# Performance work log

Measured on AMD Instinct MI355X. Metric: run time of the kernel, lower is better.

## Reference

```python
import jax, jax.numpy as jnp
import numpy as np
from jax import lax

WEIGHT = 1.0
NUM_DILATION_STEPS = 20
FAR_DIST = 20.0


def _neighbor_count(x, kernel, num_classes):
    # grouped 3x3 conv with center tap zeroed, SAME padding (stride 1)
    return lax.conv_general_dilated(
        x, kernel, window_strides=(1, 1), padding='SAME',
        feature_group_count=num_classes,
        dimension_numbers=('NCHW', 'OIHW', 'NCHW'))


def fast_sdf(target_mask, num_classes):
    # target_mask: [B, H, W] int labels -> per-class chamfer-ish distance map [B, C, H, W]
    one_hot = jnp.transpose(jax.nn.one_hot(target_mask, num_classes, dtype=jnp.float32),
                            (0, 3, 1, 2))  # [B, C, H, W]
    foreground = (one_hot > 0.5).astype(jnp.float32)

    # 3x3 all-ones kernel with center zero, one per class (grouped conv)
    k = np.ones((num_classes, 1, 3, 3), dtype=np.float32)
    k[:, 0, 1, 1] = 0.0
    kernel = jnp.asarray(k)

    dist_map0 = jnp.zeros_like(foreground)

    def step(i, state):
        dist_map, current_mask = state
        dilated = (_neighbor_count(current_mask, kernel, num_classes) > 0).astype(jnp.float32)
        # note: faithful to torch code -- pixels with no neighbors vanish and
        # contribute negative increments, exactly as `dilated - current_mask` does
        new_pixels = dilated - current_mask
        dist_map = dist_map + new_pixels * (i + 1).astype(jnp.float32)
        return (dist_map, dilated)

    dist_map, current_mask = lax.fori_loop(0, NUM_DILATION_STEPS, step,
                                           (dist_map0, foreground))
    return jnp.where(current_mask == 0, FAR_DIST, dist_map)


def setup_inputs() -> dict:
    key = jax.random.key(0)
    k1, k2 = jax.random.split(key)
    B, C, H, W = 8, 19, 512, 512
    pred = jax.random.normal(k1, (B, C, H, W), dtype=jnp.float32)
    target = jax.random.randint(k2, (B, H, W), 0, C, dtype=jnp.int64)
    return {"pred": pred, "target": target}


def reference(pred, target):
    num_classes = pred.shape[1]
    probs = jax.nn.softmax(pred, axis=1)
    gt_sdf = lax.stop_gradient(fast_sdf(target, num_classes))
    loss = jnp.mean(probs * gt_sdf)
    return WEIGHT * loss
```

## Files before the change

### kernel.cpp

```cpp
#include <hip/hip_runtime.h>

#define B_ 8
#define C_ 19
#define H_ 512
#define W_ 512
#define HW_ (H_*W_)

#define HALO   20
#define INTR   8
#define WIN    48
#define NSTRIP 64

typedef unsigned long long u64;

__global__ __launch_bounds__(256) void mask_kernel(const int* __restrict__ target,
                                                   u64* __restrict__ masks) {
    __shared__ u64 mlds[64][21];
    const int blk  = blockIdx.x;
    const int b    = blk >> 6;
    const int base = (blk & 63) * 64;
    const int tid  = threadIdx.x;
    const int lane = tid & 63, wv = tid >> 6;
    const int* tgt = target + b * HW_;
    for (int t = 0; t < 16; ++t) {
        const int cl = wv * 16 + t;
        const int x  = tgt[(base + cl) * 64 + lane];
        u64 keep = 0;
        #pragma unroll
        for (int c = 0; c < C_; ++c) {
            u64 m = __ballot(x == c);
            if (lane == c) keep = m;
        }
        if (lane < C_) mlds[cl][lane] = keep;
    }
    __syncthreads();
    for (int idx = tid; idx < C_ * 64; idx += 256) {
        const int c = idx >> 6, wl = idx & 63;
        masks[((size_t)b * C_ + c) * 4096 + base + wl] = mlds[wl][c];
    }
}

__global__ __launch_bounds__(256, 2) void fused_kernel(const u64* __restrict__ masks,
                                                       const float* __restrict__ pred,
                                                       float* __restrict__ out) {
    __shared__ unsigned char sdfl[C_ * INTR * W_];
    __shared__ float part[4];
    const int blk   = blockIdx.x;
    const int strip = blk & 63;
    const int b     = blk >> 6;
    const int tid   = threadIdx.x;
    const int wv    = tid >> 6, lane = tid & 63;
    const int w     = lane & 7, g = lane >> 3;
    const int gytop = strip * INTR - HALO;

    for (int c = wv; c < C_; c += 4) {
        const u64* mk = masks + ((size_t)b * C_ + c) * 4096;
        u64 cov[6], h[6], iso[6], pl[6][5];

        #pragma unroll
        for (int i = 0; i < 6; ++i) {
            const int gy = gytop + g * 6 + i;
            cov[i] = (gy >= 0 && gy < H_) ? mk[gy * 8 + w] : 0;
            iso[i] = 0;
            #pragma unroll
            for (int j = 0; j < 5; ++j) pl[i][j] = 0;
        }

        u64 nc[6];
        {
            unsigned mp = 0, lp = 0;
            #pragma unroll
            for (int i = 0; i < 6; ++i) {
                mp |= (unsigned)(cov[i] >> 63) << i;
                lp |= ((unsigned)cov[i] & 1) << i;
            }
            unsigned fl = __shfl_up(mp, 1);   if (w == 0) fl = 0;
            unsigned fr = __shfl_down(lp, 1); if (w == 7) fr = 0;
            #pragma unroll
            for (int i = 0; i < 6; ++i) {
                nc[i] = (cov[i] << 1) | (cov[i] >> 1) | (u64)((fl >> i) & 1) | ((u64)((fr >> i) & 1) << 63);
                h[i]  = nc[i] | cov[i];
            }
        }

        bool active;
        {
            u64 hup = __shfl_up(h[5], 8);   if (g == 0) hup = 0;
            u64 hdn = __shfl_down(h[0], 8); if (g == 7) hdn = 0;
            u64 d[6], diffw = 0;
            #pragma unroll
            for (int i = 0; i < 6; ++i) {
                const u64 up  = (i > 0) ? h[i - 1] : hup;
                const u64 dn  = (i < 5) ? h[i + 1] : hdn;
                const u64 nbr = nc[i] | up | dn;
                iso[i] = cov[i] & ~nbr;
                const u64 nb = nbr & ~cov[i];
                pl[i][0] = nb;
                d[i] = cov[i] | nbr;
                diffw |= nb;
                cov[i] = d[i];
            }
            unsigned mp = 0, lp = 0;
            #pragma unroll
            for (int i = 0; i < 6; ++i) {
                mp |= (unsigned)(cov[i] >> 63) << i;
                lp |= ((unsigned)cov[i] & 1) << i;
            }
            unsigned fl = __shfl_up(mp, 1);   if (w == 0) fl = 0;
            unsigned fr = __shfl_down(lp, 1); if (w == 7) fr = 0;
            #pragma unroll
            for (int i = 0; i < 6; ++i)
                h[i] = cov[i] | (cov[i] << 1) | (cov[i] >> 1) | (u64)((fl >> i) & 1) | ((u64)((fr >> i) & 1) << 63);
            active = __any(diffw != 0);
        }

        if (active) {
            #pragma unroll
            for (int s = 2; s <= 19; ++s) {
                u64 hup = __shfl_up(h[5], 8);   if (g == 0) hup = 0;
                u64 hdn = __shfl_down(h[0], 8); if (g == 7) hdn = 0;
                u64 diffw = 0;
                #pragma unroll
                for (int i = 0; i < 6; ++i) {
                    const u64 up = (i > 0) ? h[i - 1] : hup;
                    const u64 dn = (i < 5) ? h[i + 1] : hdn;
                    const u64 d  = up | h[i] | dn;
                    const u64 nb = d ^ cov[i];
                    diffw |= nb;
                    if (s & 1)  pl[i][0] |= nb;
                    if (s & 2)  pl[i][1] |= nb;
                    if (s & 4)  pl[i][2] |= nb;
                    if (s & 8)  pl[i][3] |= nb;
                    if (s & 16) pl[i][4] |= nb;
                    cov[i] = d;
                }
                if (!__any(diffw != 0)) break;
                if (s < 19) {
                    unsigned mp = 0, lp = 0;
                    #pragma unroll
                    for (int i = 0; i < 6; ++i) {
                        mp |= (unsigned)(cov[i] >> 63) << i;
                        lp |= ((unsigned)cov[i] & 1) << i;
                    }
                    unsigned fl = __shfl_up(mp, 1);   if (w == 0) fl = 0;
                    unsigned fr = __shfl_down(lp, 1); if (w == 7) fr = 0;
                    #pragma unroll
                    for (int i = 0; i < 6; ++i)
                        h[i] = cov[i] | (cov[i] << 1) | (cov[i] >> 1) | (u64)((fl >> i) & 1) | ((u64)((fr >> i) & 1) << 63);
                }
            }
        }

        #pragma unroll
        for (int i = 0; i < 6; ++i) {
            const int lr = g * 6 + i;
            if (lr < HALO || lr >= HALO + INTR) continue;
            pl[i][0] |= iso[i];
            const u64 m = ~cov[i];
            pl[i][2] |= m;
            pl[i][4] |= m;
            u64* dst = (u64*)&sdfl[(c * INTR + (lr - HALO)) * W_ + w * 64];
            #pragma unroll
            for (int g2 = 0; g2 < 8; ++g2) {
                u64 x = 0;
                #pragma unroll
                for (int j = 0; j < 5; ++j)
                    x |= ((pl[i][j] >> (8 * g2)) & 0xFFULL) << (8 * j);
                u64 t;
                t = (x ^ (x >> 7))  & 0x00AA00AA00AA00AAULL; x ^= t ^ (t << 7);
                t = (x ^ (x >> 14)) & 0x0000CCCC0000CCCCULL; x ^= t ^ (t << 14);
                t = (x ^ (x >> 28)) & 0x00000000F0F0F0F0ULL; x ^= t ^ (t << 28);
                dst[g2] = x;
            }
        }
    }
    __syncthreads();

    float acc = 0.f;
    const float* pb = pred + (size_t)b * C_ * HW_ + (size_t)strip * INTR * W_;
    #pragma unroll
    for (int k = 0; k < 4; ++k) {
        const int p = k * 1024 + tid * 4;
        float4 den = {0.f, 0.f, 0.f, 0.f};
        float4 num = {0.f, 0.f, 0.f, 0.f};
        #pragma unroll
        for (int c = 0; c < C_; ++c) {
            const float4 v  = *(const float4*)(pb + (size_t)c * HW_ + p);
            const uchar4 sv = *(const uchar4*)&sdfl[c * 4096 + p];
            const float e0 = __expf(v.x), e1 = __expf(v.y);
            const float e2 = __expf(v.z), e3 = __expf(v.w);
            den.x += e0; den.y += e1; den.z += e2; den.w += e3;
            num.x = fmaf(e0, (float)sv.x, num.x);
            num.y = fmaf(e1, (float)sv.y, num.y);
            num.z = fmaf(e2, (float)sv.z, num.z);
            num.w = fmaf(e3, (float)sv.w, num.w);
        }
        acc += num.x / den.x + num.y / den.y + num.z / den.z + num.w / den.w;
    }

    #pragma unroll
    for (int off = 32; off > 0; off >>= 1) acc += __shfl_down(acc, off);
    if ((tid & 63) == 0) part[tid >> 6] = acc;
    __syncthreads();
    if (tid == 0) {
        float s = (part[0] + part[1]) + (part[2] + part[3]);
        atomicAdd(out, s * (1.0f / 39845888.0f));
    }
}

extern "C" void kernel_launch(void* const* d_in, const int* in_sizes, int n_in,
                              void* d_out, int out_size, void* d_ws, size_t ws_size,
                              hipStream_t stream) {
    const float* pred   = (const float*)d_in[0];
    const int*   target = (const int*)d_in[1];
    u64* masks = (u64*)d_ws;
    float* out = (float*)d_out;

    hipMemsetAsync(out, 0, sizeof(float), stream);
    mask_kernel<<<512, 256, 0, stream>>>(target, masks);
    fused_kernel<<<B_ * NSTRIP, 256, 0, stream>>>(masks, pred, out);
}
```

Measured before the change: 277.4 us.

## Split fused dilation+loss kernel into separate dilate and loss kernels

New measurement: 300.2 us. 8.2% more time.

```diff
diff --git a/kernel.cpp b/kernel.cpp
--- a/kernel.cpp
+++ b/kernel.cpp
@@ -8,7 +8,6 @@
 
 #define HALO   20
 #define INTR   8
-#define WIN    48
 #define NSTRIP 64
 
 typedef unsigned long long u64;
@@ -40,169 +39,161 @@
     }
 }
 
-__global__ __launch_bounds__(256, 2) void fused_kernel(const u64* __restrict__ masks,
-                                                       const float* __restrict__ pred,
-                                                       float* __restrict__ out) {
-    __shared__ unsigned char sdfl[C_ * INTR * W_];
-    __shared__ float part[4];
-    const int blk   = blockIdx.x;
-    const int strip = blk & 63;
-    const int b     = blk >> 6;
-    const int tid   = threadIdx.x;
-    const int wv    = tid >> 6, lane = tid & 63;
+__global__ __launch_bounds__(256) void dilate_kernel(const u64* __restrict__ masks,
+                                                     unsigned char* __restrict__ sdf) {
+    const int wid   = blockIdx.x * 4 + (threadIdx.x >> 6);
+    const int strip = wid & 63;
+    const int bc    = wid >> 6;
+    const int lane  = threadIdx.x & 63;
     const int w     = lane & 7, g = lane >> 3;
     const int gytop = strip * INTR - HALO;
-
-    for (int c = wv; c < C_; c += 4) {
-        const u64* mk = masks + ((size_t)b * C_ + c) * 4096;
-        u64 cov[6], h[6], iso[6], pl[6][5];
-
-        #pragma unroll
-        for (int i = 0; i < 6; ++i) {
-            const int gy = gytop + g * 6 + i;
-            cov[i] = (gy >= 0 && gy < H_) ? mk[gy * 8 + w] : 0;
-            iso[i] = 0;
-            #pragma unroll
-            for (int j = 0; j < 5; ++j) pl[i][j] = 0;
-        }
-
+    const u64* mk   = masks + (size_t)bc * 4096;
+
+    u64 cov[6], h[6], pl[6][5];
+    #pragma unroll
+    for (int i = 0; i < 6; ++i) {
+        const int gy = gytop + g * 6 + i;
+        cov[i] = (gy >= 0 && gy < H_) ? mk[gy * 8 + w] : 0;
+        #pragma unroll
+        for (int j = 0; j < 5; ++j) pl[i][j] = 0;
+    }
+
+    bool active;
+    {
         u64 nc[6];
-        {
-            unsigned mp = 0, lp = 0;
+        unsigned mp = 0, lp = 0;
+        #pragma unroll
+        for (int i = 0; i < 6; ++i) {
+            mp |= (unsigned)(cov[i] >> 63) << i;
+            lp |= ((unsigned)cov[i] & 1) << i;
+        }
+        unsigned fl = __shfl_up(mp, 1);   if (w == 0) fl = 0;
+        unsigned fr = __shfl_down(lp, 1); if (w == 7) fr = 0;
+        #pragma unroll
+        for (int i = 0; i < 6; ++i) {
+            nc[i] = (cov[i] << 1) | (cov[i] >> 1) | (u64)((fl >> i) & 1) | ((u64)((fr >> i) & 1) << 63);
+            h[i]  = nc[i] | cov[i];
+        }
+        u64 hup = __shfl_up(h[5], 8);   if (g == 0) hup = 0;
+        u64 hdn = __shfl_down(h[0], 8); if (g == 7) hdn = 0;
+        u64 diffw = 0;
+        #pragma unroll
+        for (int i = 0; i < 6; ++i) {
+            const u64 up  = (i > 0) ? h[i - 1] : hup;
+            const u64 dn  = (i < 5) ? h[i + 1] : hdn;
+            const u64 nbr = nc[i] | up | dn;
+            const u64 nb  = nbr & ~cov[i];
+            pl[i][0] = nb | (cov[i] & ~nbr);
+            diffw |= nb;
+            cov[i] |= nbr;
+        }
+        mp = 0; lp = 0;
+        #pragma unroll
+        for (int i = 0; i < 6; ++i) {
+            mp |= (unsigned)(cov[i] >> 63) << i;
+            lp |= ((unsigned)cov[i] & 1) << i;
+        }
+        fl = __shfl_up(mp, 1);   if (w == 0) fl = 0;
+        fr = __shfl_down(lp, 1); if (w == 7) fr = 0;
+        #pragma unroll
+        for (int i = 0; i < 6; ++i)
+            h[i] = cov[i] | (cov[i] << 1) | (cov[i] >> 1) | (u64)((fl >> i) & 1) | ((u64)((fr >> i) & 1) << 63);
+        active = __any(diffw != 0);
+    }
+
+    if (active) {
+        #pragma unroll
+        for (int s = 2; s <= 19; ++s) {
+            u64 hup = __shfl_up(h[5], 8);   if (g == 0) hup = 0;
+            u64 hdn = __shfl_down(h[0], 8); if (g == 7) hdn = 0;
+            u64 diffw = 0;
             #pragma unroll
             for (int i = 0; i < 6; ++i) {
-                mp |= (unsigned)(cov[i] >> 63) << i;
-                lp |= ((unsigned)cov[i] & 1) << i;
+                const u64 up = (i > 0) ? h[i - 1] : hup;
+                const u64 dn = (i < 5) ? h[i + 1] : hdn;
+                const u64 d  = up | h[i] | dn;
+                const u64 nb = d ^ cov[i];
+                diffw |= nb;
+                if (s & 1)  pl[i][0] |= nb;
+                if (s & 2)  pl[i][1] |= nb;
+                if (s & 4)  pl[i][2] |= nb;
+                if (s & 8)  pl[i][3] |= nb;
+                if (s & 16) pl[i][4] |= nb;
+                cov[i] = d;
             }
-            unsigned fl = __shfl_up(mp, 1);   if (w == 0) fl = 0;
-            unsigned fr = __shfl_down(lp, 1); if (w == 7) fr = 0;
-            #pragma unroll
-            for (int i = 0; i < 6; ++i) {
-                nc[i] = (cov[i] << 1) | (cov[i] >> 1) | (u64)((fl >> i) & 1) | ((u64)((fr >> i) & 1) << 63);
-                h[i]  = nc[i] | cov[i];
-            }
-        }
-
-        bool active;
-        {
-            u64 hup = __shfl_up(h[5], 8);   if (g == 0) hup = 0;
-            u64 hdn = __shfl_down(h[0], 8); if (g == 7) hdn = 0;
-            u64 d[6], diffw = 0;
-            #pragma unroll
-            for (int i = 0; i < 6; ++i) {
-                const u64 up  = (i > 0) ? h[i - 1] : hup;
-                const u64 dn  = (i < 5) ? h[i + 1] : hdn;
-                const u64 nbr = nc[i] | up | dn;
-                iso[i] = cov[i] & ~nbr;
-                const u64 nb = nbr & ~cov[i];
-                pl[i][0] = nb;
-                d[i] = cov[i] | nbr;
-                diffw |= nb;
-                cov[i] = d[i];
-            }
-            unsigned mp = 0, lp = 0;
-            #pragma unroll
-            for (int i = 0; i < 6; ++i) {
-                mp |= (unsigned)(cov[i] >> 63) << i;
-                lp |= ((unsigned)cov[i] & 1) << i;
-            }
-            unsigned fl = __shfl_up(mp, 1);   if (w == 0) fl = 0;
-            unsigned fr = __shfl_down(lp, 1); if (w == 7) fr = 0;
-            #pragma unroll
-            for (int i = 0; i < 6; ++i)
-                h[i] = cov[i] | (cov[i] << 1) | (cov[i] >> 1) | (u64)((fl >> i) & 1) | ((u64)((fr >> i) & 1) << 63);
-            active = __any(diffw != 0);
-        }
-
-        if (active) {
-            #pragma unroll
-            for (int s = 2; s <= 19; ++s) {
-                u64 hup = __shfl_up(h[5], 8);   if (g == 0) hup = 0;
-                u64 hdn = __shfl_down(h[0], 8); if (g == 7) hdn = 0;
-                u64 diffw = 0;
+            if (!__any(diffw != 0)) break;
+            if (s < 19) {
+                unsigned mp = 0, lp = 0;
                 #pragma unroll
                 for (int i = 0; i < 6; ++i) {
-                    const u64 up = (i > 0) ? h[i - 1] : hup;
-                    const u64 dn = (i < 5) ? h[i + 1] : hdn;
-                    const u64 d  = up | h[i] | dn;
-                    const u64 nb = d ^ cov[i];
-                    diffw |= nb;
-                    if (s & 1)  pl[i][0] |= nb;
-                    if (s & 2)  pl[i][1] |= nb;
-                    if (s & 4)  pl[i][2] |= nb;
-                    if (s & 8)  pl[i][3] |= nb;
-                    if (s & 16) pl[i][4] |= nb;
-                    cov[i] = d;
+                    mp |= (unsigned)(cov[i] >> 63) << i;
+                    lp |= ((unsigned)cov[i] & 1) << i;
                 }
-                if (!__any(diffw != 0)) break;
-                if (s < 19) {
-                    unsigned mp = 0, lp = 0;
-                    #pragma unroll
-                    for (int i = 0; i < 6; ++i) {
-                        mp |= (unsigned)(cov[i] >> 63) << i;
-                        lp |= ((unsigned)cov[i] & 1) << i;
-                    }
-                    unsigned fl = __shfl_up(mp, 1);   if (w == 0) fl = 0;
-                    unsigned fr = __shfl_down(lp, 1); if (w == 7) fr = 0;
-                    #pragma unroll
-                    for (int i = 0; i < 6; ++i)
-                        h[i] = cov[i] | (cov[i] << 1) | (cov[i] >> 1) | (u64)((fl >> i) & 1) | ((u64)((fr >> i) & 1) << 63);
-                }
+                unsigned fl = __shfl_up(mp, 1);   if (w == 0) fl = 0;
+                unsigned fr = __shfl_down(lp, 1); if (w == 7) fr = 0;
+                #pragma unroll
+                for (int i = 0; i < 6; ++i)
+                    h[i] = cov[i] | (cov[i] << 1) | (cov[i] >> 1) | (u64)((fl >> i) & 1) | ((u64)((fr >> i) & 1) << 63);
             }
         }
-
-        #pragma unroll
-        for (int i = 0; i < 6; ++i) {
-            const int lr = g * 6 + i;
-            if (lr < HALO || lr >= HALO + INTR) continue;
-            pl[i][0] |= iso[i];
-            const u64 m = ~cov[i];
-            pl[i][2] |= m;
-            pl[i][4] |= m;
-            u64* dst = (u64*)&sdfl[(c * INTR + (lr - HALO)) * W_ + w * 64];
+    }
+
+    #pragma unroll
+    for (int i = 0; i < 6; ++i) {
+        const int lr = g * 6 + i;
+        if (lr < HALO || lr >= HALO + INTR) continue;
+        const int gy = gytop + lr;
+        const u64 m = ~cov[i];
+        pl[i][2] |= m;
+        pl[i][4] |= m;
+        union { u64 q[8]; uint4 v[4]; } o;
+        #pragma unroll
+        for (int g2 = 0; g2 < 8; ++g2) {
+            u64 x = 0;
             #pragma unroll
-            for (int g2 = 0; g2 < 8; ++g2) {
-                u64 x = 0;
-                #pragma unroll
-                for (int j = 0; j < 5; ++j)
-                    x |= ((pl[i][j] >> (8 * g2)) & 0xFFULL) << (8 * j);
-                u64 t;
-                t = (x ^ (x >> 7))  & 0x00AA00AA00AA00AAULL; x ^= t ^ (t << 7);
-                t = (x ^ (x >> 14)) & 0x0000CCCC0000CCCCULL; x ^= t ^ (t << 14);
-                t = (x ^ (x >> 28)) & 0x00000000F0F0F0F0ULL; x ^= t ^ (t << 28);
-                dst[g2] = x;
-            }
-        }
-    }
+            for (int j = 0; j < 5; ++j)
+                x |= ((pl[i][j] >> (8 * g2)) & 0xFFULL) << (8 * j);
+            u64 t;
+            t = (x ^ (x >> 7))  & 0x00AA00AA00AA00AAULL; x ^= t ^ (t << 7);
+            t = (x ^ (x >> 14)) & 0x0000CCCC0000CCCCULL; x ^= t ^ (t << 14);
+            t = (x ^ (x >> 28)) & 0x00000000F0F0F0F0ULL; x ^= t ^ (t << 28);
+            o.q[g2] = x;
+        }
+        uint4* dst = (uint4*)(sdf + (size_t)bc * HW_ + gy * W_ + w * 64);
+        #pragma unroll
+        for (int k = 0; k < 4; ++k) dst[k] = o.v[k];
+    }
+}
+
+__global__ __launch_bounds__(256) void loss_kernel(const float* __restrict__ pred,
+                                                   const unsigned char* __restrict__ sdf,
+                                                   float* __restrict__ out) {
+    const int t   = blockIdx.x * 256 + threadIdx.x;
+    const int b   = t >> 16;
+    const int hw4 = (t & 65535) << 2;
+    const float*         pbase = pred + (size_t)b * C_ * HW_ + hw4;
+    const unsigned char* sbase = sdf  + (size_t)b * C_ * HW_ + hw4;
+    float4 den = {0.f, 0.f, 0.f, 0.f};
+    float4 num = {0.f, 0.f, 0.f, 0.f};
+    #pragma unroll
+    for (int c = 0; c < C_; ++c) {
+        const float4 v  = *(const float4*)(pbase + (size_t)c * HW_);
+        const uchar4 sv = *(const uchar4*)(sbase + (size_t)c * HW_);
+        const float e0 = __expf(v.x), e1 = __expf(v.y);
+        const float e2 = __expf(v.z), e3 = __expf(v.w);
+        den.x += e0; den.y += e1; den.z += e2; den.w += e3;
+        num.x = fmaf(e0, (float)sv.x, num.x);
+        num.y = fmaf(e1, (float)sv.y, num.y);
+        num.z = fmaf(e2, (float)sv.z, num.z);
+        num.w = fmaf(e3, (float)sv.w, num.w);
+    }
+    float acc = num.x / den.x + num.y / den.y + num.z / den.z + num.w / den.w;
+    #pragma unroll
+    for (int off = 32; off > 0; off >>= 1) acc += __shfl_down(acc, off);
+    __shared__ float part[4];
+    if ((threadIdx.x & 63) == 0) part[threadIdx.x >> 6] = acc;
     __syncthreads();
-
-    float acc = 0.f;
-    const float* pb = pred + (size_t)b * C_ * HW_ + (size_t)strip * INTR * W_;
-    #pragma unroll
-    for (int k = 0; k < 4; ++k) {
-        const int p = k * 1024 + tid * 4;
-        float4 den = {0.f, 0.f, 0.f, 0.f};
-        float4 num = {0.f, 0.f, 0.f, 0.f};
-        #pragma unroll
-        for (int c = 0; c < C_; ++c) {
-            const float4 v  = *(const float4*)(pb + (size_t)c * HW_ + p);
-            const uchar4 sv = *(const uchar4*)&sdfl[c * 4096 + p];
-            const float e0 = __expf(v.x), e1 = __expf(v.y);
-            const float e2 = __expf(v.z), e3 = __expf(v.w);
-            den.x += e0; den.y += e1; den.z += e2; den.w += e3;
-            num.x = fmaf(e0, (float)sv.x, num.x);
-            num.y = fmaf(e1, (float)sv.y, num.y);
-            num.z = fmaf(e2, (float)sv.z, num.z);
-            num.w = fmaf(e3, (float)sv.w, num.w);
-        }
-        acc += num.x / den.x + num.y / den.y + num.z / den.z + num.w / den.w;
-    }
-
-    #pragma unroll
-    for (int off = 32; off > 0; off >>= 1) acc += __shfl_down(acc, off);
-    if ((tid & 63) == 0) part[tid >> 6] = acc;
-    __syncthreads();
-    if (tid == 0) {
+    if (threadIdx.x == 0) {
         float s = (part[0] + part[1]) + (part[2] + part[3]);
         atomicAdd(out, s * (1.0f / 39845888.0f));
     }
@@ -214,9 +205,11 @@
     const float* pred   = (const float*)d_in[0];
     const int*   target = (const int*)d_in[1];
     u64* masks = (u64*)d_ws;
+    unsigned char* sdf = (unsigned char*)d_ws + 4980736;
     float* out = (float*)d_out;
 
     hipMemsetAsync(out, 0, sizeof(float), stream);
     mask_kernel<<<512, 256, 0, stream>>>(target, masks);
-    fused_kernel<<<B_ * NSTRIP, 256, 0, stream>>>(masks, pred, out);
-}
+    dilate_kernel<<<B_ * C_ * NSTRIP / 4, 256, 0, stream>>>(masks, sdf);
+    loss_kernel<<<2048, 256, 0, stream>>>(pred, sdf, out);
+}
```
